# Optimization experiments

Measured on AMD Instinct MI355X. Metric: run time of the kernel, lower is better.

## Reference

```python
import jax, jax.numpy as jnp
import numpy as np

B, H, W, C = 32, 56, 56, 384
WS, SS, NH = 7, 3, 12
HD = C // NH
SCALE = HD ** -0.5
N = WS * WS
NW = (H // WS) * (W // WS)
HIDDEN = 4 * C
EPS = 1e-5


def _rel_pos_index():
    coords = np.stack(np.meshgrid(np.arange(WS), np.arange(WS), indexing='ij')).reshape(2, -1)
    rel = coords[:, :, None] - coords[:, None, :]
    rel = rel.transpose(1, 2, 0).astype(np.int64)
    rel[..., 0] += WS - 1
    rel[..., 1] += WS - 1
    rel[..., 0] *= 2 * WS - 1
    return rel.sum(-1)  # [N, N]


def _attn_mask():
    img = np.zeros((H, W), dtype=np.float32)
    slices = (slice(0, -WS), slice(-WS, -SS), slice(-SS, None))
    cnt = 0
    for hs in slices:
        for ws_ in slices:
            img[hs, ws_] = cnt
            cnt += 1
    mw = img.reshape(H // WS, WS, W // WS, WS).transpose(0, 2, 1, 3).reshape(-1, N)  # [nW, N]
    am = mw[:, None, :] - mw[:, :, None]
    return np.where(am != 0, -100.0, 0.0).astype(np.float32)  # [nW, N, N]


REL_IDX = jnp.asarray(_rel_pos_index())
ATTN_MASK = jnp.asarray(_attn_mask())


def _ln(x, g, b):
    mu = x.mean(-1, keepdims=True)
    var = ((x - mu) ** 2).mean(-1, keepdims=True)
    return (x - mu) * jax.lax.rsqrt(var + EPS) * g + b


def setup_inputs() -> dict:
    key = jax.random.key(0)
    ks = jax.random.split(key, 16)
    s = 0.02
    return {
        'x': jax.random.normal(ks[0], (B, H * W, C), jnp.float32),
        'norm1_g': jnp.ones((C,), jnp.float32),
        'norm1_b': jnp.zeros((C,), jnp.float32),
        'qkv_w': jax.random.normal(ks[1], (C, 3 * C), jnp.float32) * s,
        'qkv_b': jnp.zeros((3 * C,), jnp.float32),
        'bias_table': jax.random.normal(ks[2], ((2 * WS - 1) ** 2, NH), jnp.float32) * s,
        'proj_w': jax.random.normal(ks[3], (C, C), jnp.float32) * s,
        'proj_b': jnp.zeros((C,), jnp.float32),
        'norm2_g': jnp.ones((C,), jnp.float32),
        'norm2_b': jnp.zeros((C,), jnp.float32),
        'fc1_w': jax.random.normal(ks[4], (C, HIDDEN), jnp.float32) * s,
        'fc1_b': jnp.zeros((HIDDEN,), jnp.float32),
        'fc2_w': jax.random.normal(ks[5], (HIDDEN, C), jnp.float32) * s,
        'fc2_b': jnp.zeros((C,), jnp.float32),
    }


def reference(x, norm1_g, norm1_b, qkv_w, qkv_b, bias_table, proj_w, proj_b,
              norm2_g, norm2_b, fc1_w, fc1_b, fc2_w, fc2_b):
    shortcut = x
    h = _ln(x, norm1_g, norm1_b).reshape(B, H, W, C)
    # cyclic shift
    h = jnp.roll(h, shift=(-SS, -SS), axis=(1, 2))
    # window partition -> [B*nW, N, C]
    hw = h.reshape(B, H // WS, WS, W // WS, WS, C).transpose(0, 1, 3, 2, 4, 5).reshape(-1, N, C)
    Bw = hw.shape[0]
    # qkv
    qkv = (hw @ qkv_w + qkv_b).reshape(Bw, N, 3, NH, HD).transpose(2, 0, 3, 1, 4)
    q, k, v = qkv[0] * SCALE, qkv[1], qkv[2]  # [Bw, NH, N, HD]
    attn = jnp.einsum('whnd,whmd->whnm', q, k)
    rel_bias = bias_table[REL_IDX.reshape(-1)].reshape(N, N, NH).transpose(2, 0, 1)
    attn = attn + rel_bias[None]
    # shift mask: [Bw] = [B, nW]
    attn = attn.reshape(B, NW, NH, N, N) + ATTN_MASK[None, :, None]
    attn = jax.nn.softmax(attn.reshape(Bw, NH, N, N), axis=-1)
    o = jnp.einsum('whnm,whmd->whnd', attn, v).transpose(0, 2, 1, 3).reshape(Bw, N, C)
    o = o @ proj_w + proj_b
    # window reverse + reverse shift
    o = o.reshape(B, H // WS, W // WS, WS, WS, C).transpose(0, 1, 3, 2, 4, 5).reshape(B, H, W, C)
    o = jnp.roll(o, shift=(SS, SS), axis=(1, 2)).reshape(B, H * W, C)
    x = shortcut + o
    # MLP
    m = _ln(x, norm2_g, norm2_b)
    m = jax.nn.gelu(m @ fc1_w + fc1_b, approximate=False)
    m = m @ fc2_w + fc2_b
    return x + m
```

## Files before the change

kernel.cpp:

```cpp
#include <hip/hip_runtime.h>
#include <hip/hip_bf16.h>
#include <cstdint>
#include <cstddef>

static constexpr int Bv  = 32;
static constexpr int Cv  = 384;
static constexpr int Nv  = 49;
static constexpr int Mv  = 32 * 64 * 49;
static constexpr float SCALEv = 0.17677669529663687f;

using bf16 = __hip_bfloat16;
typedef __bf16 bf16x8 __attribute__((ext_vector_type(8)));
typedef float  f32x4  __attribute__((ext_vector_type(4)));

__global__ __launch_bounds__(256)
void wt_kernel(const float* __restrict__ w, bf16* __restrict__ wt, int K, int N) {
    int idx = blockIdx.x * 256 + threadIdx.x;
    if (idx >= K * N) return;
    int n = idx / K, k = idx - n * K;
    wt[idx] = (bf16)w[(size_t)k * N + n];
}

__global__ __launch_bounds__(256)
void bm_kernel(const float* __restrict__ btab, float* __restrict__ bmt) {
    const int cls = blockIdx.x, h = blockIdx.y;
    for (int idx = threadIdx.x; idx < 4096; idx += 256) {
        int q = idx >> 6, k = idx & 63;
        float v;
        if (k >= 49) {
            v = -1e30f;
        } else {
            int n = q < 49 ? q : 48;
            int m = k;
            int i1 = n / 7, j1 = n - i1 * 7;
            int i2 = m / 7, j2 = m - i2 * 7;
            v = btab[((i1 - i2 + 6) * 13 + (j1 - j2 + 6)) * 12 + h];
            int lh1 = (cls & 2) ? (i1 < 4 ? 1 : 2) : 0;
            int lw1 = (cls & 1) ? (j1 < 4 ? 1 : 2) : 0;
            int lh2 = (cls & 2) ? (i2 < 4 ? 1 : 2) : 0;
            int lw2 = (cls & 1) ? (j2 < 4 ? 1 : 2) : 0;
            if ((lh1 * 3 + lw1) != (lh2 * 3 + lw2)) v += -100.f;
        }
        bmt[((size_t)(cls * 12 + h) * 64 + q) * 64 + k] = v;
    }
}

template <int MODE>
__global__ __launch_bounds__(256)
void ln_kernel(const float* __restrict__ src, const float* __restrict__ gam,
               const float* __restrict__ bet, bf16* __restrict__ dst) {
    const int wave = threadIdx.x >> 6, lane = threadIdx.x & 63;
    const int r = blockIdx.x * 4 + wave;
    size_t srow;
    if (MODE == 0) {
        int w  = r / 49, n = r - w * 49;
        int b  = w >> 6, win = w & 63;
        int hb = win >> 3, wb = win & 7;
        int ii = n / 7, jj = n - ii * 7;
        int hh = hb * 7 + ii + 3; if (hh >= 56) hh -= 56;
        int ww = wb * 7 + jj + 3; if (ww >= 56) ww -= 56;
        srow = (size_t)b * 3136 + hh * 56 + ww;
    } else {
        srow = (size_t)r;
    }
    const float* p = src + srow * 384;
    float vals[6];
    float s = 0.f, s2 = 0.f;
#pragma unroll
    for (int t = 0; t < 6; ++t) {
        float v = p[t * 64 + lane];
        vals[t] = v; s += v; s2 += v * v;
    }
#pragma unroll
    for (int o = 32; o > 0; o >>= 1) {
        s  += __shfl_xor(s,  o, 64);
        s2 += __shfl_xor(s2, o, 64);
    }
    const float mu  = s * (1.f / 384.f);
    const float var = s2 * (1.f / 384.f) - mu * mu;
    const float rs  = rsqrtf(var + 1e-5f);
    bf16* q = dst + (size_t)r * 384;
#pragma unroll
    for (int t = 0; t < 6; ++t) {
        int e = t * 64 + lane;
        q[e] = (bf16)((vals[t] - mu) * rs * gam[e] + bet[e]);
    }
}

__global__ __launch_bounds__(64)
void attn_kernel(const bf16* __restrict__ qkv, const float* __restrict__ bmt,
                 bf16* __restrict__ o) {
    const int w = blockIdx.x;
    const int h = blockIdx.y;
    const int lane = threadIdx.x;
    const int quad = lane >> 4, l16 = lane & 15;
    __shared__ bf16 Vt[32][72];
    __shared__ bf16 Ps[64][72];

    const size_t rowbase = (size_t)w * 49;

    for (int idx = lane; idx < 49 * 16; idx += 64) {
        int row = idx >> 4, dp = (idx & 15) << 1;
        const bf16* src = qkv + (rowbase + row) * 1152 + 768 + h * 32 + dp;
        Vt[dp][row]     = src[0];
        Vt[dp + 1][row] = src[1];
    }
    for (int idx = lane; idx < 512; idx += 64) {
        int d = idx >> 4, c = idx & 15;
        if (c) Vt[d][48 + c] = (bf16)0.f;
    }

    f32x4 acc[4][4] = {};
    bf16x8 kf[4], qf[4];
#pragma unroll
    for (int i = 0; i < 4; ++i) {
        int row = 16 * i + l16; if (row > 48) row = 48;
        kf[i] = *(const bf16x8*)(qkv + (rowbase + row) * 1152 + 384 + h * 32 + quad * 8);
    }
#pragma unroll
    for (int j = 0; j < 4; ++j) {
        int row = 16 * j + l16; if (row > 48) row = 48;
        qf[j] = *(const bf16x8*)(qkv + (rowbase + row) * 1152 + h * 32 + quad * 8);
    }
#pragma unroll
    for (int i = 0; i < 4; ++i)
#pragma unroll
        for (int j = 0; j < 4; ++j)
            acc[i][j] = __builtin_amdgcn_mfma_f32_16x16x32_bf16(kf[i], qf[j], acc[i][j], 0, 0, 0);

    const int cls = (((w & 63) >= 56) ? 2 : 0) + (((w & 7) == 7) ? 1 : 0);
    const float* bmbase = bmt + (size_t)(cls * 12 + h) * 4096;
#pragma unroll
    for (int j = 0; j < 4; ++j) {
        f32x4 bm[4];
#pragma unroll
        for (int i = 0; i < 4; ++i)
            bm[i] = *(const f32x4*)(bmbase + (16 * j + l16) * 64 + 16 * i + quad * 4);
        float s[4][4];
        float mx = -3.0e38f;
#pragma unroll
        for (int i = 0; i < 4; ++i)
#pragma unroll
            for (int t = 0; t < 4; ++t) {
                s[i][t] = acc[i][j][t] + bm[i][t];
                mx = fmaxf(mx, s[i][t]);
            }
        mx = fmaxf(mx, __shfl_xor(mx, 16, 64));
        mx = fmaxf(mx, __shfl_xor(mx, 32, 64));
        float p[4][4];
        float sum = 0.f;
#pragma unroll
        for (int i = 0; i < 4; ++i)
#pragma unroll
            for (int t = 0; t < 4; ++t) {
                p[i][t] = __expf(s[i][t] - mx);
                sum += p[i][t];
            }
        sum += __shfl_xor(sum, 16, 64);
        sum += __shfl_xor(sum, 32, 64);
        const float inv = 1.f / sum;
#pragma unroll
        for (int i = 0; i < 4; ++i) {
            bf16 pk[4];
#pragma unroll
            for (int t = 0; t < 4; ++t) pk[t] = (bf16)(p[i][t] * inv);
            *(uint64_t*)(&Ps[16 * j + l16][16 * i + 4 * quad]) = *(const uint64_t*)pk;
        }
    }
    __syncthreads();

    f32x4 oacc[4][2] = {};
    bf16x8 vb[2][2];
#pragma unroll
    for (int jn = 0; jn < 2; ++jn)
#pragma unroll
        for (int ks = 0; ks < 2; ++ks)
            vb[jn][ks] = *(const bf16x8*)(&Vt[16 * jn + l16][32 * ks + quad * 8]);
#pragma unroll
    for (int i = 0; i < 4; ++i) {
#pragma unroll
        for (int ks = 0; ks < 2; ++ks) {
            bf16x8 pa = *(const bf16x8*)(&Ps[16 * i + l16][32 * ks + quad * 8]);
#pragma unroll
            for (int jn = 0; jn < 2; ++jn)
                oacc[i][jn] = __builtin_amdgcn_mfma_f32_16x16x32_bf16(pa, vb[jn][ks], oacc[i][jn], 0, 0, 0);
        }
    }

#pragma unroll
    for (int i = 0; i < 4; ++i) {
        int nbase = 16 * i + quad * 4;
#pragma unroll
        for (int t = 0; t < 4; ++t) {
            int n = nbase + t;
            if (n < 49) {
                bf16* dst = o + (rowbase + n) * 384 + h * 32;
                dst[l16]      = (bf16)(oacc[i][0][t]);
                dst[16 + l16] = (bf16)(oacc[i][1][t]);
            }
        }
    }
}

template <int EPI>
__global__ __launch_bounds__(256, 3)
void gemm_bt(const bf16* __restrict__ A, const bf16* __restrict__ Bt,
             const float* __restrict__ bias, int N, int K,
             bf16* __restrict__ outb, float* __restrict__ outf,
             const float* __restrict__ resid) {
    __shared__ bf16 As[128 * 64];
    __shared__ bf16 Bs[128 * 64];
    const int tid  = threadIdx.x;
    const int lane = tid & 63, wave = tid >> 6;
    const int quad = lane >> 4, l16 = lane & 15;
    const int wm = wave >> 1, wn = wave & 1;

    const int nbx = gridDim.x;
    const int nwg = nbx * (int)gridDim.y;
    const int ord = (int)blockIdx.y * nbx + (int)blockIdx.x;
    const int cpx = nwg >> 3;
    const int work = (ord & 7) * cpx + (ord >> 3);
    const int by = work / nbx;
    const int bx = work - by * nbx;
    const long m0 = (long)by * 128;
    const long n0 = (long)bx * 128;

    f32x4 acc[4][4] = {};
    const int nk = K >> 6;

    const bf16* aG[4];
    const bf16* bG[4];
    int wOff[4];
#pragma unroll
    for (int it = 0; it < 4; ++it) {
        int e   = it * 256 + tid;
        int row = e >> 3, c = e & 7;
        aG[it]   = A  + (size_t)(m0 + row) * K + (c << 3);
        bG[it]   = Bt + (size_t)(n0 + row) * K + (c << 3);
        wOff[it] = (row * 8 + (c ^ (row & 7))) * 8;
    }

    bf16x8 rA[4], rB[4];
    auto ldg = [&](int k0) {
#pragma unroll
        for (int it = 0; it < 4; ++it) {
            rA[it] = *(const bf16x8*)(aG[it] + k0);
            rB[it] = *(const bf16x8*)(bG[it] + k0);
        }
    };
    auto dsw = [&]() {
#pragma unroll
        for (int it = 0; it < 4; ++it) {
            *(bf16x8*)(As + wOff[it]) = rA[it];
            *(bf16x8*)(Bs + wOff[it]) = rB[it];
        }
    };

    ldg(0);
    dsw();
    __syncthreads();

    const int sxA = (l16 & 7);
    for (int kt = 0; kt < nk; ++kt) {
        const bool more = (kt + 1 < nk);
        if (more) ldg((kt + 1) * 64);
#pragma unroll
        for (int kk = 0; kk < 64; kk += 32) {
            const int cs = quad + (kk >> 3);
            const int so = ((cs ^ sxA) << 3);
            bf16x8 af[4], bfr[4];
#pragma unroll
            for (int i = 0; i < 4; ++i)
                af[i] = *(const bf16x8*)(As + (wm * 64 + i * 16 + l16) * 64 + so);
#pragma unroll
            for (int j = 0; j < 4; ++j)
                bfr[j] = *(const bf16x8*)(Bs + (wn * 64 + j * 16 + l16) * 64 + so);
#pragma unroll
            for (int i = 0; i < 4; ++i)
#pragma unroll
                for (int j = 0; j < 4; ++j)
                    acc[i][j] = __builtin_amdgcn_mfma_f32_16x16x32_bf16(af[i], bfr[j], acc[i][j], 0, 0, 0);
        }
        if (more) {
            __syncthreads();
            dsw();
            __syncthreads();
        }
    }

#pragma unroll
    for (int i = 0; i < 4; ++i) {
        const long mbase = m0 + wm * 64 + i * 16 + quad * 4;
#pragma unroll
        for (int j = 0; j < 4; ++j) {
            const int col = (int)n0 + wn * 64 + j * 16 + l16;
            const float bv = bias[col];
            f32x4 r = acc[i][j];
#pragma unroll
            for (int t = 0; t < 4; ++t) {
                const long m = mbase + t;
                float val = r[t] + bv;
                if constexpr (EPI == 0) {
                    float sc = (col < 384) ? SCALEv : 1.0f;
                    outb[(size_t)m * N + col] = (bf16)(val * sc);
                } else if constexpr (EPI == 1) {
                    int w  = (int)(m / 49), n = (int)(m - (long)w * 49);
                    int b  = w >> 6, win = w & 63;
                    int hb = win >> 3, wb = win & 7;
                    int ii = n / 7, jj = n - ii * 7;
                    int hh = hb * 7 + ii + 3; if (hh >= 56) hh -= 56;
                    int ww = wb * 7 + jj + 3; if (ww >= 56) ww -= 56;
                    size_t dst = ((size_t)b * 3136 + hh * 56 + ww) * 384 + col;
                    outf[dst] = resid[dst] + val;
                } else if constexpr (EPI == 2) {
                    float g = 0.5f * val * (1.0f + erff(val * 0.70710678118654752f));
                    outb[(size_t)m * N + col] = (bf16)g;
                } else {
                    size_t oo = (size_t)m * N + col;
                    outf[oo] = resid[oo] + val;
                }
            }
        }
    }
}

extern "C" void kernel_launch(void* const* d_in, const int* in_sizes, int n_in,
                              void* d_out, int out_size, void* d_ws, size_t ws_size,
                              hipStream_t stream) {
    const float* x     = (const float*)d_in[0];
    const float* n1g   = (const float*)d_in[1];
    const float* n1b   = (const float*)d_in[2];
    const float* qkvw  = (const float*)d_in[3];
    const float* qkvb  = (const float*)d_in[4];
    const float* btab  = (const float*)d_in[5];
    const float* projw = (const float*)d_in[6];
    const float* projb = (const float*)d_in[7];
    const float* n2g   = (const float*)d_in[8];
    const float* n2b   = (const float*)d_in[9];
    const float* fc1w  = (const float*)d_in[10];
    const float* fc1b  = (const float*)d_in[11];
    const float* fc2w  = (const float*)d_in[12];
    const float* fc2b  = (const float*)d_in[13];
    float* out = (float*)d_out;

    char* ws = (char*)d_ws;
    size_t off = 0;
    auto take = [&](size_t bytes) {
        char* p = ws + off;
        off += (bytes + 255) & ~(size_t)255;
        return p;
    };
    bf16* qkv_wt  = (bf16*)take((size_t)1152 * 384 * 2);
    bf16* proj_wt = (bf16*)take((size_t)384 * 384 * 2);
    bf16* fc1_wt  = (bf16*)take((size_t)1536 * 384 * 2);
    bf16* fc2_wt  = (bf16*)take((size_t)384 * 1536 * 2);
    float* bmt    = (float*)take((size_t)4 * 12 * 64 * 64 * 4);
    bf16* qkv_buf = (bf16*)take((size_t)Mv * 1152 * 2);
    bf16* o_buf   = (bf16*)take((size_t)Mv * 384 * 2);
    bf16* hw_buf  = (bf16*)take((size_t)Mv * 384 * 2);
    float* x1     = (float*)take((size_t)Mv * 384 * 4);
    bf16* g_buf   = qkv_buf;
    bf16* x1n     = hw_buf;

    wt_kernel<<<(384 * 1152 + 255) / 256, 256, 0, stream>>>(qkvw,  qkv_wt,  384, 1152);
    wt_kernel<<<(384 * 384  + 255) / 256, 256, 0, stream>>>(projw, proj_wt, 384, 384);
    wt_kernel<<<(384 * 1536 + 255) / 256, 256, 0, stream>>>(fc1w,  fc1_wt,  384, 1536);
    wt_kernel<<<(1536 * 384 + 255) / 256, 256, 0, stream>>>(fc2w,  fc2_wt,  1536, 384);
    bm_kernel<<<dim3(4, 12), 256, 0, stream>>>(btab, bmt);
    ln_kernel<0><<<Mv / 4, 256, 0, stream>>>(x, n1g, n1b, hw_buf);
    gemm_bt<0><<<dim3(1152 / 128, Mv / 128), 256, 0, stream>>>(
        hw_buf, qkv_wt, qkvb, 1152, 384, qkv_buf, nullptr, nullptr);
    attn_kernel<<<dim3(2048, 12), 64, 0, stream>>>(qkv_buf, bmt, o_buf);
    gemm_bt<1><<<dim3(384 / 128, Mv / 128), 256, 0, stream>>>(
        o_buf, proj_wt, projb, 384, 384, nullptr, x1, x);
    ln_kernel<1><<<Mv / 4, 256, 0, stream>>>(x1, n2g, n2b, x1n);
    gemm_bt<2><<<dim3(1536 / 128, Mv / 128), 256, 0, stream>>>(
        x1n, fc1_wt, fc1b, 1536, 384, g_buf, nullptr, nullptr);
    gemm_bt<3><<<dim3(384 / 128, Mv / 128), 256, 0, stream>>>(
        g_buf, fc2_wt, fc2b, 384, 1536, nullptr, out, x1);
}
```

Measured before the change: 1.134 ms.

## Split window attention across four waves, one per 16-row query tile

The attention kernel now launches 256 threads per (window, head) block instead of one 64-lane wave. Each wave owns one 16-row query tile: it computes its QK^T strip, softmax and PV product independently, while all waves share the V-transpose staging. This raises per-block parallelism and cuts per-thread register pressure. The cost is that every wave reloads all K fragments, and the fourth wave handles mostly padded rows (49 of 64 are real).

```diff
diff --git a/kernel.cpp b/kernel.cpp
--- a/kernel.cpp
+++ b/kernel.cpp
@@ -87,117 +87,103 @@
     }
 }
 
-__global__ __launch_bounds__(64)
+__global__ __launch_bounds__(256, 4)
 void attn_kernel(const bf16* __restrict__ qkv, const float* __restrict__ bmt,
                  bf16* __restrict__ o) {
     const int w = blockIdx.x;
     const int h = blockIdx.y;
-    const int lane = threadIdx.x;
+    const int tid  = threadIdx.x;
+    const int wv   = tid >> 6;
+    const int lane = tid & 63;
     const int quad = lane >> 4, l16 = lane & 15;
     __shared__ bf16 Vt[32][72];
     __shared__ bf16 Ps[64][72];
 
     const size_t rowbase = (size_t)w * 49;
 
-    for (int idx = lane; idx < 49 * 16; idx += 64) {
+    for (int idx = tid; idx < 512; idx += 256) {
+        int d = idx >> 4, c = idx & 15;
+        if (c) Vt[d][48 + c] = (bf16)0.f;
+    }
+    for (int idx = tid; idx < 49 * 16; idx += 256) {
         int row = idx >> 4, dp = (idx & 15) << 1;
         const bf16* src = qkv + (rowbase + row) * 1152 + 768 + h * 32 + dp;
         Vt[dp][row]     = src[0];
         Vt[dp + 1][row] = src[1];
     }
-    for (int idx = lane; idx < 512; idx += 64) {
-        int d = idx >> 4, c = idx & 15;
-        if (c) Vt[d][48 + c] = (bf16)0.f;
-    }
-
-    f32x4 acc[4][4] = {};
-    bf16x8 kf[4], qf[4];
+
+    f32x4 acc[4] = {};
+    bf16x8 kf[4], qf;
 #pragma unroll
     for (int i = 0; i < 4; ++i) {
         int row = 16 * i + l16; if (row > 48) row = 48;
         kf[i] = *(const bf16x8*)(qkv + (rowbase + row) * 1152 + 384 + h * 32 + quad * 8);
     }
-#pragma unroll
-    for (int j = 0; j < 4; ++j) {
-        int row = 16 * j + l16; if (row > 48) row = 48;
-        qf[j] = *(const bf16x8*)(qkv + (rowbase + row) * 1152 + h * 32 + quad * 8);
+    {
+        int row = 16 * wv + l16; if (row > 48) row = 48;
+        qf = *(const bf16x8*)(qkv + (rowbase + row) * 1152 + h * 32 + quad * 8);
     }
 #pragma unroll
     for (int i = 0; i < 4; ++i)
-#pragma unroll
-        for (int j = 0; j < 4; ++j)
-            acc[i][j] = __builtin_amdgcn_mfma_f32_16x16x32_bf16(kf[i], qf[j], acc[i][j], 0, 0, 0);
+        acc[i] = __builtin_amdgcn_mfma_f32_16x16x32_bf16(kf[i], qf, acc[i], 0, 0, 0);
 
     const int cls = (((w & 63) >= 56) ? 2 : 0) + (((w & 7) == 7) ? 1 : 0);
     const float* bmbase = bmt + (size_t)(cls * 12 + h) * 4096;
-#pragma unroll
-    for (int j = 0; j < 4; ++j) {
-        f32x4 bm[4];
-#pragma unroll
-        for (int i = 0; i < 4; ++i)
-            bm[i] = *(const f32x4*)(bmbase + (16 * j + l16) * 64 + 16 * i + quad * 4);
-        float s[4][4];
-        float mx = -3.0e38f;
-#pragma unroll
-        for (int i = 0; i < 4; ++i)
-#pragma unroll
-            for (int t = 0; t < 4; ++t) {
-                s[i][t] = acc[i][j][t] + bm[i][t];
-                mx = fmaxf(mx, s[i][t]);
-            }
-        mx = fmaxf(mx, __shfl_xor(mx, 16, 64));
-        mx = fmaxf(mx, __shfl_xor(mx, 32, 64));
-        float p[4][4];
-        float sum = 0.f;
-#pragma unroll
-        for (int i = 0; i < 4; ++i)
-#pragma unroll
-            for (int t = 0; t < 4; ++t) {
-                p[i][t] = __expf(s[i][t] - mx);
-                sum += p[i][t];
-            }
-        sum += __shfl_xor(sum, 16, 64);
-        sum += __shfl_xor(sum, 32, 64);
-        const float inv = 1.f / sum;
-#pragma unroll
-        for (int i = 0; i < 4; ++i) {
-            bf16 pk[4];
-#pragma unroll
-            for (int t = 0; t < 4; ++t) pk[t] = (bf16)(p[i][t] * inv);
-            *(uint64_t*)(&Ps[16 * j + l16][16 * i + 4 * quad]) = *(const uint64_t*)pk;
-        }
+    f32x4 bm[4];
+#pragma unroll
+    for (int i = 0; i < 4; ++i)
+        bm[i] = *(const f32x4*)(bmbase + (16 * wv + l16) * 64 + 16 * i + quad * 4);
+    float s[4][4];
+    float mx = -3.0e38f;
+#pragma unroll
+    for (int i = 0; i < 4; ++i)
+#pragma unroll
+        for (int t = 0; t < 4; ++t) {
+            s[i][t] = acc[i][t] + bm[i][t];
+            mx = fmaxf(mx, s[i][t]);
+        }
+    mx = fmaxf(mx, __shfl_xor(mx, 16, 64));
+    mx = fmaxf(mx, __shfl_xor(mx, 32, 64));
+    float p[4][4];
+    float sum = 0.f;
+#pragma unroll
+    for (int i = 0; i < 4; ++i)
+#pragma unroll
+        for (int t = 0; t < 4; ++t) {
+            p[i][t] = __expf(s[i][t] - mx);
+            sum += p[i][t];
+        }
+    sum += __shfl_xor(sum, 16, 64);
+    sum += __shfl_xor(sum, 32, 64);
+    const float inv = 1.f / sum;
+#pragma unroll
+    for (int i = 0; i < 4; ++i) {
+        bf16 pk[4];
+#pragma unroll
+        for (int t = 0; t < 4; ++t) pk[t] = (bf16)(p[i][t] * inv);
+        *(uint64_t*)(&Ps[16 * wv + l16][16 * i + 4 * quad]) = *(const uint64_t*)pk;
     }
     __syncthreads();
 
-    f32x4 oacc[4][2] = {};
-    bf16x8 vb[2][2];
-#pragma unroll
-    for (int jn = 0; jn < 2; ++jn)
-#pragma unroll
-        for (int ks = 0; ks < 2; ++ks)
-            vb[jn][ks] = *(const bf16x8*)(&Vt[16 * jn + l16][32 * ks + quad * 8]);
-#pragma unroll
-    for (int i = 0; i < 4; ++i) {
-#pragma unroll
-        for (int ks = 0; ks < 2; ++ks) {
-            bf16x8 pa = *(const bf16x8*)(&Ps[16 * i + l16][32 * ks + quad * 8]);
-#pragma unroll
-            for (int jn = 0; jn < 2; ++jn)
-                oacc[i][jn] = __builtin_amdgcn_mfma_f32_16x16x32_bf16(pa, vb[jn][ks], oacc[i][jn], 0, 0, 0);
-        }
-    }
-
-#pragma unroll
-    for (int i = 0; i < 4; ++i) {
-        int nbase = 16 * i + quad * 4;
-#pragma unroll
-        for (int t = 0; t < 4; ++t) {
-            int n = nbase + t;
-            if (n < 49) {
-                bf16* dst = o + (rowbase + n) * 384 + h * 32;
-                dst[l16]      = (bf16)(oacc[i][0][t]);
-                dst[16 + l16] = (bf16)(oacc[i][1][t]);
-            }
+    f32x4 oacc[2] = {};
+#pragma unroll
+    for (int ks = 0; ks < 2; ++ks) {
+        bf16x8 pa = *(const bf16x8*)(&Ps[16 * wv + l16][32 * ks + quad * 8]);
+#pragma unroll
+        for (int jn = 0; jn < 2; ++jn) {
+            bf16x8 vb = *(const bf16x8*)(&Vt[16 * jn + l16][32 * ks + quad * 8]);
+            oacc[jn] = __builtin_amdgcn_mfma_f32_16x16x32_bf16(pa, vb, oacc[jn], 0, 0, 0);
+        }
+    }
+
+    const int nbase = 16 * wv + quad * 4;
+#pragma unroll
+    for (int t = 0; t < 4; ++t) {
+        int n = nbase + t;
+        if (n < 49) {
+            bf16* dst = o + (rowbase + n) * 384 + h * 32;
+            dst[l16]      = (bf16)(oacc[0][t]);
+            dst[16 + l16] = (bf16)(oacc[1][t]);
         }
     }
 }
@@ -370,7 +356,7 @@
     ln_kernel<0><<<Mv / 4, 256, 0, stream>>>(x, n1g, n1b, hw_buf);
     gemm_bt<0><<<dim3(1152 / 128, Mv / 128), 256, 0, stream>>>(
         hw_buf, qkv_wt, qkvb, 1152, 384, qkv_buf, nullptr, nullptr);
-    attn_kernel<<<dim3(2048, 12), 64, 0, stream>>>(qkv_buf, bmt, o_buf);
+    attn_kernel<<<dim3(2048, 12), 256, 0, stream>>>(qkv_buf, bmt, o_buf);
     gemm_bt<1><<<dim3(384 / 128, Mv / 128), 256, 0, stream>>>(
         o_buf, proj_wt, projb, 384, 384, nullptr, x1, x);
     ln_kernel<1><<<Mv / 4, 256, 0, stream>>>(x1, n2g, n2b, x1n);
```

After: 1.124 ms. About the same (-0.9%).
